# Kernel optimization log

Measured on AMD Instinct MI355X. Metric: run time of the kernel, lower is better.

## Reference

```python
import jax, jax.numpy as jnp
import numpy as np

HEADS = 16
DIM_HEAD = 64
SCALE = DIM_HEAD ** -0.5


def setup_inputs() -> dict:
    key = jax.random.key(0)
    ks = jax.random.split(key, 7)
    b, n, m, d = 2, 2048, 2048, 1024
    inner = HEADS * DIM_HEAD  # 1024
    patch_embed = jax.random.normal(ks[0], (b, n, d), dtype=jnp.float32)
    pixel_embed = jax.random.normal(ks[1], (b, m, d), dtype=jnp.float32)
    s = 1.0 / np.sqrt(d)
    Wq = jax.random.normal(ks[2], (d, inner), dtype=jnp.float32) * s
    Wk = jax.random.normal(ks[3], (d, inner), dtype=jnp.float32) * s
    Wv = jax.random.normal(ks[4], (d, inner), dtype=jnp.float32) * s
    Wo = jax.random.normal(ks[5], (inner, d), dtype=jnp.float32) * (1.0 / np.sqrt(inner))
    bo = jax.random.normal(ks[6], (d,), dtype=jnp.float32) * 0.01
    return {"patch_embed": patch_embed, "pixel_embed": pixel_embed,
            "Wq": Wq, "Wk": Wk, "Wv": Wv, "Wo": Wo, "bo": bo}


def reference(patch_embed, pixel_embed, Wq, Wk, Wv, Wo, bo):
    b, n, _ = patch_embed.shape
    h, dh = HEADS, DIM_HEAD
    # projections
    q = patch_embed @ Wq  # [b, n, h*dh]
    k = pixel_embed @ Wk  # [b, m, h*dh]
    v = pixel_embed @ Wv  # [b, m, h*dh]
    # split heads: [b, seq, h, dh]
    q = q.reshape(b, n, h, dh)
    k = k.reshape(b, -1, h, dh)
    v = v.reshape(b, -1, h, dh)
    sim = jnp.einsum('bihd,bjhd->bhij', q, k) * SCALE  # [b, h, n, m]
    attn = jax.nn.softmax(sim, axis=-1)
    out = jnp.einsum('bhij,bjhd->bihd', attn, v)  # [b, n, h, dh]
    out = out.reshape(b, n, h * dh)
    return out @ Wo + bo  # [b, n, query_dim]
```

## Files before the change

### kernel.cpp

```cpp
#include <hip/hip_runtime.h>

#define SEQ 2048
#define DMODEL 1024
#define HEADS 16
#define DH 64
#define QSCALE 0.180336880f

typedef __attribute__((ext_vector_type(8))) short short8;
typedef __attribute__((ext_vector_type(4))) float f32x4;
typedef __attribute__((ext_vector_type(16))) float f32x16;
typedef __attribute__((ext_vector_type(2))) unsigned int uint2v;
typedef __attribute__((ext_vector_type(4))) unsigned int uint4v;

__device__ __forceinline__ ushort f2bf(float x) {
  union { float f; unsigned u; } v; v.f = x;
  return (ushort)((v.u + 0x7fffu + ((v.u >> 16) & 1u)) >> 16);
}

__device__ __forceinline__ void gld16(const ushort* g, ushort* l) {
  __builtin_amdgcn_global_load_lds(
      (const __attribute__((address_space(1))) unsigned int*)g,
      (__attribute__((address_space(3))) unsigned int*)l, 16, 0, 0);
}

__global__ __launch_bounds__(256) void prologue(
    const float* __restrict__ patch, const float* __restrict__ pixel,
    const float* __restrict__ W0, const float* __restrict__ W1,
    const float* __restrict__ W2, const float* __restrict__ W3,
    ushort* __restrict__ pb, ushort* __restrict__ xb,
    ushort* __restrict__ O0, ushort* __restrict__ O1,
    ushort* __restrict__ O2, ushort* __restrict__ O3) {
  const int z = blockIdx.z;
  const int tx = threadIdx.x, ty = threadIdx.y;
  if (z < 2) {
    const float4* in = (const float4*)(z ? pixel : patch);
    ushort4* out = (ushort4*)(z ? xb : pb);
    const int base = (blockIdx.y * 32 + blockIdx.x) * 256 + ty * 32 + tx;
#pragma unroll
    for (int rep = 0; rep < 4; ++rep) {
      const int i = base + rep * 262144;
      float4 f = in[i];
      out[i] = make_ushort4(f2bf(f.x), f2bf(f.y), f2bf(f.z), f2bf(f.w));
    }
    return;
  }
  __shared__ float tile[32][33];
  const int zz = z - 2;
  const float* in = zz == 0 ? W0 : zz == 1 ? W1 : zz == 2 ? W2 : W3;
  ushort* out = zz == 0 ? O0 : zz == 1 ? O1 : zz == 2 ? O2 : O3;
  const float scale = zz == 0 ? QSCALE : 1.0f;
  const int n0 = blockIdx.x * 32, k0 = blockIdx.y * 32;
#pragma unroll
  for (int i = 0; i < 4; ++i)
    tile[ty + i * 8][tx] = in[(size_t)(k0 + ty + i * 8) * DMODEL + n0 + tx];
  __syncthreads();
#pragma unroll
  for (int i = 0; i < 4; ++i)
    out[(size_t)(n0 + ty + i * 8) * DMODEL + k0 + tx] =
        f2bf(tile[tx][ty + i * 8] * scale);
}

__global__ __launch_bounds__(256) void mfma_gemm_qkv(
    const ushort* __restrict__ pb, const ushort* __restrict__ xb,
    const ushort* __restrict__ wqt, const ushort* __restrict__ wkt,
    const ushort* __restrict__ wvt, ushort* __restrict__ qws,
    ushort* __restrict__ kws, ushort* __restrict__ vws) {
  __shared__ __align__(16) ushort As[128 * 64];
  __shared__ __align__(16) ushort Bs[128 * 64];
  const int z = blockIdx.z;
  const ushort* A = (z == 0) ? pb : xb;
  const ushort* Bt = (z == 0) ? wqt : (z == 1) ? wkt : wvt;

  const int t = threadIdx.x;
  const int w = t >> 6, lane = t & 63, ln = lane & 15, q = lane >> 4;
  const int wm = w & 1, wn = w >> 1;
  const int row0 = blockIdx.y * 128, col0 = blockIdx.x * 128;
  const int sw = ln & 7;

  f32x4 acc[4][4];
#pragma unroll
  for (int i = 0; i < 4; ++i)
#pragma unroll
    for (int j = 0; j < 4; ++j) acc[i][j] = (f32x4){0.f, 0.f, 0.f, 0.f};

  for (int k0 = 0; k0 < DMODEL; k0 += 64) {
    __syncthreads();
#pragma unroll
    for (int rep = 0; rep < 4; ++rep) {
      const int u0 = rep * 256 + w * 64;
      const int u = u0 + lane;
      const int r = u >> 3, gl = (u & 7) ^ (r & 7);
      gld16(&A[(size_t)(row0 + r) * DMODEL + k0 + gl * 8], &As[u0 * 8]);
      gld16(&Bt[(size_t)(col0 + r) * DMODEL + k0 + gl * 8], &Bs[u0 * 8]);
    }
    __syncthreads();
#pragma unroll
    for (int ks = 0; ks < 2; ++ks) {
      short8 af[4], bf[4];
#pragma unroll
      for (int rt = 0; rt < 4; ++rt)
        af[rt] = *(const short8*)&As[(wm * 64 + rt * 16 + ln) * 64 +
                                     (((ks * 4 + q) ^ sw) * 8)];
#pragma unroll
      for (int ct = 0; ct < 4; ++ct)
        bf[ct] = *(const short8*)&Bs[(wn * 64 + ct * 16 + ln) * 64 +
                                     (((ks * 4 + q) ^ sw) * 8)];
#pragma unroll
      for (int rt = 0; rt < 4; ++rt)
#pragma unroll
        for (int ct = 0; ct < 4; ++ct)
          acc[rt][ct] = __builtin_amdgcn_mfma_f32_16x16x32_bf16(af[rt], bf[ct],
                                                                acc[rt][ct], 0, 0, 0);
    }
  }

  if (z < 2) {
    ushort* dst = z == 0 ? qws : kws;
#pragma unroll
    for (int rt = 0; rt < 4; ++rt)
#pragma unroll
      for (int ct = 0; ct < 4; ++ct) {
        const int c = col0 + wn * 64 + ct * 16 + ln;
#pragma unroll
        for (int reg = 0; reg < 4; ++reg) {
          const int r = row0 + wm * 64 + rt * 16 + q * 4 + reg;
          dst[(size_t)r * DMODEL + c] = f2bf(acc[rt][ct][reg]);
        }
      }
  } else {
#pragma unroll
    for (int rt = 0; rt < 4; ++rt)
#pragma unroll
      for (int ct = 0; ct < 4; ++ct) {
        const int c = col0 + wn * 64 + ct * 16 + ln;
        const int hh = c >> 6, d = c & 63;
        const int r0 = row0 + wm * 64 + rt * 16 + q * 4;
        const int bb = r0 >> 11, s0 = r0 & (SEQ - 1);
        ushort4 u4 = make_ushort4(f2bf(acc[rt][ct][0]), f2bf(acc[rt][ct][1]),
                                  f2bf(acc[rt][ct][2]), f2bf(acc[rt][ct][3]));
        *(ushort4*)&vws[((size_t)(bb * HEADS + hh) * DH + d) * SEQ + s0] = u4;
      }
  }
}

__global__ __launch_bounds__(256, 2) void flash_mfma(
    const ushort* __restrict__ Qg, const ushort* __restrict__ Kg,
    const ushort* __restrict__ Vg, ushort* __restrict__ Og) {
  __shared__ __align__(16) ushort Kst[2][64 * 64];
  __shared__ __align__(16) ushort Vst[2][64 * 64];

  const int t = threadIdx.x;
  const int w = t >> 6, lane = t & 63;
  const int l31 = lane & 31, hi = lane >> 5, l7 = lane & 7, l8 = lane >> 3;
  const int bh = blockIdx.x;
  const int qt = blockIdx.y;
  const int b = bh >> 4, h = bh & 15;

  const ushort* qrow = Qg + ((size_t)b * SEQ) * DMODEL + h * DH;
  const ushort* krow = Kg + ((size_t)b * SEQ) * DMODEL + h * DH;
  const ushort* vg = Vg + (size_t)bh * DH * SEQ;

  short8 qf[4];
#pragma unroll
  for (int ks = 0; ks < 4; ++ks)
    qf[ks] = *(const short8*)
        &qrow[(size_t)(qt * 128 + w * 32 + l31) * DMODEL + ks * 16 + hi * 8];

  f32x16 acc_o[2];
#pragma unroll
  for (int db = 0; db < 2; ++db)
#pragma unroll
    for (int e = 0; e < 16; ++e) acc_o[db][e] = 0.f;
  float l_i = 0.f;

  const int fbase = (w & 1) * 4;
  const bool isV = (w >= 2);
  const int swz = (l7 ^ l8) * 8;

  {
#pragma unroll
    for (int i = 0; i < 4; ++i) {
      const int f = fbase + i;
      if (!isV)
        gld16(&krow[(size_t)(f * 8 + l8) * DMODEL + swz], &Kst[0][f * 512]);
      else
        gld16(&vg[(size_t)(f * 8 + l8) * SEQ + swz], &Vst[0][f * 512]);
    }
  }
  __syncthreads();

  for (int kt = 0; kt < SEQ / 64; ++kt) {
    const int cur = kt & 1;
    if (kt + 1 < SEQ / 64) {
#pragma unroll
      for (int i = 0; i < 4; ++i) {
        const int f = fbase + i;
        if (!isV)
          gld16(&krow[(size_t)((kt + 1) * 64 + f * 8 + l8) * DMODEL + swz],
                &Kst[cur ^ 1][f * 512]);
        else
          gld16(&vg[(size_t)(f * 8 + l8) * SEQ + (kt + 1) * 64 + swz],
                &Vst[cur ^ 1][f * 512]);
      }
    }

    const ushort* Kc = &Kst[cur][0];
    const ushort* Vc = &Vst[cur][0];

    f32x16 accs[2];
#pragma unroll
    for (int kb = 0; kb < 2; ++kb)
#pragma unroll
      for (int e = 0; e < 16; ++e) accs[kb][e] = 0.f;
#pragma unroll
    for (int kb = 0; kb < 2; ++kb)
#pragma unroll
      for (int ks = 0; ks < 4; ++ks) {
        const short8 kf = *(const short8*)
            &Kc[(kb * 32 + l31) * 64 + (((ks * 2 + hi) ^ l7) * 8)];
        accs[kb] = __builtin_amdgcn_mfma_f32_32x32x16_bf16(kf, qf[ks],
                                                           accs[kb], 0, 0, 0);
      }

    short8 vf[4][2];
#pragma unroll
    for (int sg = 0; sg < 4; ++sg)
#pragma unroll
      for (int db = 0; db < 2; ++db)
        vf[sg][db] = *(const short8*)
            &Vc[(db * 32 + l31) * 64 + (((sg * 2 + hi) ^ l7) * 8)];

#pragma unroll
    for (int kb = 0; kb < 2; ++kb)
#pragma unroll
      for (int e = 0; e < 16; ++e) {
        const float p = __builtin_amdgcn_exp2f(accs[kb][e]);
        accs[kb][e] = p;
        l_i += p;
      }

    short8 pa[4];
#pragma unroll
    for (int kb = 0; kb < 2; ++kb) {
      unsigned wq[4][2];
#pragma unroll
      for (int o = 0; o < 4; ++o) {
        asm("v_cvt_pk_bf16_f32 %0, %1, %2"
            : "=v"(wq[o][0])
            : "v"(accs[kb][4 * o + 0]), "v"(accs[kb][4 * o + 1]));
        asm("v_cvt_pk_bf16_f32 %0, %1, %2"
            : "=v"(wq[o][1])
            : "v"(accs[kb][4 * o + 2]), "v"(accs[kb][4 * o + 3]));
      }
#pragma unroll
      for (int sl = 0; sl < 2; ++sl) {
        uint2v r02 = __builtin_amdgcn_permlane32_swap(wq[2 * sl][0],
                                                      wq[2 * sl + 1][0],
                                                      false, false);
        uint2v r13 = __builtin_amdgcn_permlane32_swap(wq[2 * sl][1],
                                                      wq[2 * sl + 1][1],
                                                      false, false);
        uint4v pk = {r02.x, r13.x, r02.y, r13.y};
        pa[kb * 2 + sl] = __builtin_bit_cast(short8, pk);
      }
    }

#pragma unroll
    for (int sg = 0; sg < 4; ++sg)
#pragma unroll
      for (int db = 0; db < 2; ++db)
        acc_o[db] = __builtin_amdgcn_mfma_f32_32x32x16_bf16(pa[sg], vf[sg][db],
                                                            acc_o[db], 0, 0, 0);

    __syncthreads();
  }

  l_i += __shfl_xor(l_i, 32);
  const float inv = 1.0f / l_i;
#pragma unroll
  for (int o = 0; o < 4; ++o)
#pragma unroll
    for (int r0 = 0; r0 < 4; ++r0) {
      const int row = o * 8 + r0 + 4 * hi;
      const float invr = __shfl(inv, row, 64);
      const int s = qt * 128 + w * 32 + row;
#pragma unroll
      for (int db = 0; db < 2; ++db)
        Og[(size_t)(b * SEQ + s) * DMODEL + h * DH + db * 32 + l31] =
            f2bf(acc_o[db][4 * o + r0] * invr);
    }
}

__global__ __launch_bounds__(256) void mfma_gemm_out(const ushort* __restrict__ A,
                                                     const ushort* __restrict__ Bt,
                                                     const float* __restrict__ bias,
                                                     float* __restrict__ dst) {
  __shared__ __align__(16) ushort As[64 * 64];
  __shared__ __align__(16) ushort Bs[128 * 64];
  const int t = threadIdx.x;
  const int w = t >> 6, lane = t & 63, ln = lane & 15, q = lane >> 4;
  const int wm = w & 1, wn = w >> 1;
  const int row0 = blockIdx.y * 64, col0 = blockIdx.x * 128;
  const int sw = ln & 7;

  f32x4 acc[2][4];
#pragma unroll
  for (int i = 0; i < 2; ++i)
#pragma unroll
    for (int j = 0; j < 4; ++j) acc[i][j] = (f32x4){0.f, 0.f, 0.f, 0.f};

  for (int k0 = 0; k0 < DMODEL; k0 += 64) {
    __syncthreads();
#pragma unroll
    for (int rep = 0; rep < 2; ++rep) {
      const int u0 = rep * 256 + w * 64;
      const int u = u0 + lane;
      const int r = u >> 3, gl = (u & 7) ^ (r & 7);
      gld16(&A[(size_t)(row0 + r) * DMODEL + k0 + gl * 8], &As[u0 * 8]);
    }
#pragma unroll
    for (int rep = 0; rep < 4; ++rep) {
      const int u0 = rep * 256 + w * 64;
      const int u = u0 + lane;
      const int r = u >> 3, gl = (u & 7) ^ (r & 7);
      gld16(&Bt[(size_t)(col0 + r) * DMODEL + k0 + gl * 8], &Bs[u0 * 8]);
    }
    __syncthreads();
#pragma unroll
    for (int ks = 0; ks < 2; ++ks) {
      short8 af[2], bf[4];
#pragma unroll
      for (int rt = 0; rt < 2; ++rt)
        af[rt] = *(const short8*)&As[(wm * 32 + rt * 16 + ln) * 64 +
                                     (((ks * 4 + q) ^ sw) * 8)];
#pragma unroll
      for (int ct = 0; ct < 4; ++ct)
        bf[ct] = *(const short8*)&Bs[(wn * 64 + ct * 16 + ln) * 64 +
                                     (((ks * 4 + q) ^ sw) * 8)];
#pragma unroll
      for (int rt = 0; rt < 2; ++rt)
#pragma unroll
        for (int ct = 0; ct < 4; ++ct)
          acc[rt][ct] = __builtin_amdgcn_mfma_f32_16x16x32_bf16(af[rt], bf[ct],
                                                                acc[rt][ct], 0, 0, 0);
    }
  }

#pragma unroll
  for (int rt = 0; rt < 2; ++rt)
#pragma unroll
    for (int ct = 0; ct < 4; ++ct) {
      const int c = col0 + wn * 64 + ct * 16 + ln;
      const float bi = bias[c];
#pragma unroll
      for (int reg = 0; reg < 4; ++reg) {
        const int r = row0 + wm * 32 + rt * 16 + q * 4 + reg;
        dst[(size_t)r * DMODEL + c] = acc[rt][ct][reg] + bi;
      }
    }
}

extern "C" void kernel_launch(void* const* d_in, const int* in_sizes, int n_in,
                              void* d_out, int out_size, void* d_ws,
                              size_t ws_size, hipStream_t stream) {
  const float* patch = (const float*)d_in[0];
  const float* pixel = (const float*)d_in[1];
  const float* Wq = (const float*)d_in[2];
  const float* Wk = (const float*)d_in[3];
  const float* Wv = (const float*)d_in[4];
  const float* Wo = (const float*)d_in[5];
  const float* bo = (const float*)d_in[6];
  float* out = (float*)d_out;

  const size_t E = (size_t)2 * SEQ * DMODEL;
  const size_t W = (size_t)DMODEL * DMODEL;
  ushort* pb  = (ushort*)d_ws;
  ushort* xb  = pb + E;
  ushort* wqt = xb + E;
  ushort* wkt = wqt + W;
  ushort* wvt = wkt + W;
  ushort* wot = wvt + W;
  ushort* qws = wot + W;
  ushort* kws = qws + E;
  ushort* vws = kws + E;
  ushort* aws = vws + E;

  prologue<<<dim3(32, 32, 6), dim3(32, 8), 0, stream>>>(
      patch, pixel, Wq, Wk, Wv, Wo, pb, xb, wqt, wkt, wvt, wot);
  mfma_gemm_qkv<<<dim3(8, 32, 3), 256, 0, stream>>>(pb, xb, wqt, wkt, wvt,
                                                    qws, kws, vws);
  flash_mfma<<<dim3(32, 16), 256, 0, stream>>>(qws, kws, vws, aws);
  mfma_gemm_out<<<dim3(8, 64), 256, 0, stream>>>(aws, wot, bo, out);
}
```

Before: 190.8 us.

## Split flash attention over two KV halves and merge partial outputs

Templates the flash attention kernel so each block can process only half of the key/value sequence, doubling the grid to 1024 blocks. Each half writes unnormalised fp32 output and its row sums to workspace. A new merge kernel adds the two partials, normalises and converts to bf16 for the output projection. The launch-bounds occupancy hint rises from 2 to 4. The aim is better GPU fill and latency hiding, at the cost of roughly 64 MB of extra fp32 traffic and one more launch. The merge simply adds partials, so it is only correct if both halves share the same softmax max reference.

Result: slower. 220.6 us (+15.6%).

```diff
diff --git a/kernel.cpp b/kernel.cpp
--- a/kernel.cpp
+++ b/kernel.cpp
@@ -143,9 +143,11 @@
   }
 }
 
-__global__ __launch_bounds__(256, 2) void flash_mfma(
+template <bool SPLIT>
+__global__ __launch_bounds__(256, 4) void flash_mfma_t(
     const ushort* __restrict__ Qg, const ushort* __restrict__ Kg,
-    const ushort* __restrict__ Vg, ushort* __restrict__ Og) {
+    const ushort* __restrict__ Vg, ushort* __restrict__ Og,
+    float* __restrict__ Op, float* __restrict__ lp) {
   __shared__ __align__(16) ushort Kst[2][64 * 64];
   __shared__ __align__(16) ushort Vst[2][64 * 64];
 
@@ -155,6 +157,8 @@
   const int bh = blockIdx.x;
   const int qt = blockIdx.y;
   const int b = bh >> 4, h = bh & 15;
+  const int NKT = SPLIT ? 16 : 32;
+  const int kt0 = SPLIT ? ((int)blockIdx.z * 16) : 0;
 
   const ushort* qrow = Qg + ((size_t)b * SEQ) * DMODEL + h * DH;
   const ushort* krow = Kg + ((size_t)b * SEQ) * DMODEL + h * DH;
@@ -177,32 +181,25 @@
   const bool isV = (w >= 2);
   const int swz = (l7 ^ l8) * 8;
 
-  {
+  auto stage = [&](int kt, int buf) {
 #pragma unroll
     for (int i = 0; i < 4; ++i) {
       const int f = fbase + i;
       if (!isV)
-        gld16(&krow[(size_t)(f * 8 + l8) * DMODEL + swz], &Kst[0][f * 512]);
+        gld16(&krow[(size_t)(kt * 64 + f * 8 + l8) * DMODEL + swz],
+              &Kst[buf][f * 512]);
       else
-        gld16(&vg[(size_t)(f * 8 + l8) * SEQ + swz], &Vst[0][f * 512]);
-    }
-  }
+        gld16(&vg[(size_t)(f * 8 + l8) * SEQ + kt * 64 + swz],
+              &Vst[buf][f * 512]);
+    }
+  };
+
+  stage(kt0, 0);
   __syncthreads();
 
-  for (int kt = 0; kt < SEQ / 64; ++kt) {
-    const int cur = kt & 1;
-    if (kt + 1 < SEQ / 64) {
-#pragma unroll
-      for (int i = 0; i < 4; ++i) {
-        const int f = fbase + i;
-        if (!isV)
-          gld16(&krow[(size_t)((kt + 1) * 64 + f * 8 + l8) * DMODEL + swz],
-                &Kst[cur ^ 1][f * 512]);
-        else
-          gld16(&vg[(size_t)(f * 8 + l8) * SEQ + (kt + 1) * 64 + swz],
-                &Vst[cur ^ 1][f * 512]);
-      }
-    }
+  for (int i = 0; i < NKT; ++i) {
+    const int kt = kt0 + i, cur = i & 1;
+    if (i + 1 < NKT) stage(kt + 1, cur ^ 1);
 
     const ushort* Kc = &Kst[cur][0];
     const ushort* Vc = &Vst[cur][0];
@@ -269,26 +266,62 @@
     for (int sg = 0; sg < 4; ++sg)
 #pragma unroll
       for (int db = 0; db < 2; ++db)
-        acc_o[db] = __builtin_amdgcn_mfma_f32_32x32x16_bf16(pa[sg], vf[sg][db],
-                                                            acc_o[db], 0, 0, 0);
+        acc_o[db] = __builtin_amdgcn_mfma_f32_32x32x16_bf16(
+            pa[sg], vf[sg][db], acc_o[db], 0, 0, 0);
 
     __syncthreads();
   }
 
   l_i += __shfl_xor(l_i, 32);
-  const float inv = 1.0f / l_i;
-#pragma unroll
-  for (int o = 0; o < 4; ++o)
-#pragma unroll
-    for (int r0 = 0; r0 < 4; ++r0) {
-      const int row = o * 8 + r0 + 4 * hi;
-      const float invr = __shfl(inv, row, 64);
-      const int s = qt * 128 + w * 32 + row;
-#pragma unroll
-      for (int db = 0; db < 2; ++db)
-        Og[(size_t)(b * SEQ + s) * DMODEL + h * DH + db * 32 + l31] =
-            f2bf(acc_o[db][4 * o + r0] * invr);
-    }
+
+  if (SPLIT) {
+    float* Ops = Op + (size_t)blockIdx.z * 2 * SEQ * DMODEL;
+#pragma unroll
+    for (int o = 0; o < 4; ++o)
+#pragma unroll
+      for (int r0 = 0; r0 < 4; ++r0) {
+        const int row = o * 8 + r0 + 4 * hi;
+        const int s = qt * 128 + w * 32 + row;
+#pragma unroll
+        for (int db = 0; db < 2; ++db)
+          Ops[((size_t)b * SEQ + s) * DMODEL + h * DH + db * 32 + l31] =
+              acc_o[db][4 * o + r0];
+      }
+    if (hi == 0)
+      lp[((size_t)blockIdx.z * 32 + bh) * SEQ + qt * 128 + w * 32 + l31] = l_i;
+  } else {
+    const float inv = 1.0f / l_i;
+#pragma unroll
+    for (int o = 0; o < 4; ++o)
+#pragma unroll
+      for (int r0 = 0; r0 < 4; ++r0) {
+        const int row = o * 8 + r0 + 4 * hi;
+        const float invr = __shfl(inv, row, 64);
+        const int s = qt * 128 + w * 32 + row;
+#pragma unroll
+        for (int db = 0; db < 2; ++db)
+          Og[(size_t)(b * SEQ + s) * DMODEL + h * DH + db * 32 + l31] =
+              f2bf(acc_o[db][4 * o + r0] * invr);
+      }
+  }
+}
+
+__global__ __launch_bounds__(256) void merge_o(const float* __restrict__ Op,
+                                               const float* __restrict__ lp,
+                                               ushort* __restrict__ aws) {
+  const int row = blockIdx.x;
+  const int c = threadIdx.x * 4;
+  const int b_ = row >> 11, s = row & 2047, h = c >> 6;
+  const float lsum = lp[(b_ * 16 + h) * SEQ + s] +
+                     lp[(size_t)32 * SEQ + (b_ * 16 + h) * SEQ + s];
+  const float inv = 1.0f / lsum;
+  const float4 o0 = *(const float4*)&Op[(size_t)row * DMODEL + c];
+  const float4 o1 =
+      *(const float4*)&Op[(size_t)2 * SEQ * DMODEL + (size_t)row * DMODEL + c];
+  ushort4 u = make_ushort4(
+      f2bf((o0.x + o1.x) * inv), f2bf((o0.y + o1.y) * inv),
+      f2bf((o0.z + o1.z) * inv), f2bf((o0.w + o1.w) * inv));
+  *(ushort4*)&aws[(size_t)row * DMODEL + c] = u;
 }
 
 __global__ __launch_bounds__(256) void mfma_gemm_out(const ushort* __restrict__ A,
@@ -384,11 +417,23 @@
   ushort* kws = qws + E;
   ushort* vws = kws + E;
   ushort* aws = vws + E;
+  const size_t base_ush = (size_t)6 * E + 4 * W;
+  float* Opart = (float*)(pb + base_ush);
+  float* lpart = Opart + (size_t)2 * 2 * SEQ * DMODEL;
+  const size_t need_bytes =
+      base_ush * 2 + ((size_t)2 * 2 * SEQ * DMODEL + 2 * 32 * SEQ) * 4;
 
   prologue<<<dim3(32, 32, 6), dim3(32, 8), 0, stream>>>(
       patch, pixel, Wq, Wk, Wv, Wo, pb, xb, wqt, wkt, wvt, wot);
   mfma_gemm_qkv<<<dim3(8, 32, 3), 256, 0, stream>>>(pb, xb, wqt, wkt, wvt,
                                                     qws, kws, vws);
-  flash_mfma<<<dim3(32, 16), 256, 0, stream>>>(qws, kws, vws, aws);
+  if (ws_size >= need_bytes) {
+    flash_mfma_t<true><<<dim3(32, 16, 2), 256, 0, stream>>>(
+        qws, kws, vws, nullptr, Opart, lpart);
+    merge_o<<<4096, 256, 0, stream>>>(Opart, lpart, aws);
+  } else {
+    flash_mfma_t<false><<<dim3(32, 16, 1), 256, 0, stream>>>(
+        qws, kws, vws, aws, nullptr, nullptr);
+  }
   mfma_gemm_out<<<dim3(8, 64), 256, 0, stream>>>(aws, wot, bo, out);
 }
```
